# Kernel tuning notes

Hardware: AMD Instinct MI355X
Metric: run time of the kernel (lower is better)

The kernel has to match this reference:

```python
import jax, jax.numpy as jnp
import numpy as np

NBIN = 256
EPS = 1e-10


def _diffhist(img, hmin, hmax):
    # Soft (linear-interpolation) histogram, faithful to torch index_add version.
    img = img.ravel()
    keep = (img >= hmin) & (img <= hmax)
    dh = (hmax - hmin) / (NBIN - 1)
    x = (img - hmin) / dh
    idx = jnp.floor(x)
    d = x - idx  # fractional part, carries the gradient
    # zero-weight + clamped index instead of boolean compaction (jit-friendly)
    idx_i = jnp.where(keep, idx.astype(jnp.int32), 0)
    w0 = jnp.where(keep, 1.0 - d, 0.0)
    w1 = jnp.where(keep, d, 0.0)
    h = jnp.zeros(NBIN + 1, dtype=img.dtype)
    h = h.at[idx_i].add(w0).at[idx_i + 1].add(w1)
    return h[:NBIN]


def setup_inputs() -> dict:
    key = jax.random.key(0)
    k0, k1 = jax.random.split(key)
    shape = (4, 256, 256, 256)
    img0 = jax.random.normal(k0, shape, dtype=jnp.float32)
    img1 = jax.random.normal(k1, shape, dtype=jnp.float32)
    return {"img0": img0, "img1": img1}


def reference(img0, img1):
    min0 = jnp.min(img0)  # differentiable, like torch.min
    h0 = _diffhist(img0, min0, 0.0)
    h1 = _diffhist(img1, min0, 0.0)
    h0 = (h0 + EPS) / (h0.sum() + EPS)
    h1 = (h1 + EPS) / (h1.sum() + EPS)
    # KLDivLoss(log_target=True, reduction='mean'):
    #   mean( exp(target) * (target - input) )
    inp = jnp.log((h1 + EPS) / h1)
    tgt = jnp.log((h1 + EPS) / h0)
    return jnp.mean(jnp.exp(tgt) * (tgt - inp))
```

## Files before the change

### kernel.cpp

```cpp
#include <hip/hip_runtime.h>

#define NBIN 256
#define EPSF 1e-10f
#define DSCALE 4096.0f
#define DSCALE_INV (1.0 / 4096.0)
#define DMASK ((1ull << 40) - 1)

__device__ __forceinline__ unsigned enc_f32(float f) {
    unsigned u = __float_as_uint(f);
    return (u & 0x80000000u) ? ~u : (u ^ 0x80000000u);
}
__device__ __forceinline__ float dec_f32(unsigned e) {
    unsigned u = (e & 0x80000000u) ? (e ^ 0x80000000u) : ~e;
    return __uint_as_float(u);
}

__global__ void init_kernel(unsigned* ws_min, unsigned long long* gh) {
    if (threadIdx.x == 0) *ws_min = 0xFFFFFFFFu;
    for (int j = threadIdx.x; j < 2 * NBIN; j += blockDim.x) gh[j] = 0ull;
}

__global__ void __launch_bounds__(256) min_kernel(const float4* __restrict__ img0,
                                                  long n4, unsigned* ws_min) {
    long stride = (long)gridDim.x * blockDim.x;
    long i = (long)blockIdx.x * blockDim.x + threadIdx.x;
    float m = __int_as_float(0x7f800000);
    if (i < n4) {
        float4 cur = img0[i];
        long j = i + stride;
        for (; j < n4; j += stride) {
            float4 nxt = img0[j];
            m = fminf(m, fminf(fminf(cur.x, cur.y), fminf(cur.z, cur.w)));
            cur = nxt;
        }
        m = fminf(m, fminf(fminf(cur.x, cur.y), fminf(cur.z, cur.w)));
    }
    for (int off = 32; off; off >>= 1) m = fminf(m, __shfl_xor(m, off));
    __shared__ float sm[4];
    int lane = threadIdx.x & 63, wid = threadIdx.x >> 6;
    if (lane == 0) sm[wid] = m;
    __syncthreads();
    if (threadIdx.x == 0) {
        float bm = fminf(fminf(sm[0], sm[1]), fminf(sm[2], sm[3]));
        atomicMin(ws_min, enc_f32(bm));
    }
}

__device__ __forceinline__ void hadd(float v, float hmin, float inv_dh,
                                     unsigned* h, int lane) {
    bool keep = (v >= hmin) & (v <= 0.f);
    float x = (v - hmin) * inv_dh;
    x = fminf(fmaxf(x, 0.f), 255.f);
    float fi = floorf(x);
    int idx = (int)fi;
    unsigned di = __float2uint_rn((x - fi) * DSCALE);
    unsigned pv = keep ? ((1u << 24) | di) : 0u;
    idx = keep ? idx : lane;
    atomicAdd(&h[idx], pv);
}

__global__ void __launch_bounds__(256) hist_kernel(const float4* __restrict__ img0,
                                                   const float4* __restrict__ img1,
                                                   long n4, const unsigned* ws_min,
                                                   unsigned long long* __restrict__ gh) {
    __shared__ unsigned lh[4][2][NBIN];
    int tid = threadIdx.x;
    int wid = tid >> 6;
    int lane = tid & 63;
    unsigned* base = &lh[0][0][0];
    for (int j = tid; j < 4 * 2 * NBIN; j += 256) base[j] = 0u;
    __syncthreads();

    float hmin = dec_f32(*ws_min);
    float dh = (0.f - hmin) / (NBIN - 1);
    float inv_dh = 1.0f / dh;

    long stride = (long)gridDim.x * blockDim.x;
    unsigned* h0 = &lh[wid][0][0];
    unsigned* h1 = &lh[wid][1][0];

    long i = (long)blockIdx.x * blockDim.x + tid;
    if (i < n4) {
        float4 a = img0[i];
        float4 b = img1[i];
        long j = i + stride;
        for (; j < n4; j += stride) {
            float4 an = img0[j];
            float4 bn = img1[j];
            hadd(a.x, hmin, inv_dh, h0, lane);
            hadd(a.y, hmin, inv_dh, h0, lane);
            hadd(a.z, hmin, inv_dh, h0, lane);
            hadd(a.w, hmin, inv_dh, h0, lane);
            hadd(b.x, hmin, inv_dh, h1, lane);
            hadd(b.y, hmin, inv_dh, h1, lane);
            hadd(b.z, hmin, inv_dh, h1, lane);
            hadd(b.w, hmin, inv_dh, h1, lane);
            a = an;
            b = bn;
        }
        hadd(a.x, hmin, inv_dh, h0, lane);
        hadd(a.y, hmin, inv_dh, h0, lane);
        hadd(a.z, hmin, inv_dh, h0, lane);
        hadd(a.w, hmin, inv_dh, h0, lane);
        hadd(b.x, hmin, inv_dh, h1, lane);
        hadd(b.y, hmin, inv_dh, h1, lane);
        hadd(b.z, hmin, inv_dh, h1, lane);
        hadd(b.w, hmin, inv_dh, h1, lane);
    }
    __syncthreads();

    for (int b = tid; b < NBIN; b += 256) {
        unsigned long long c0 = 0, f0 = 0, c1 = 0, f1 = 0;
        for (int w = 0; w < 4; ++w) {
            unsigned p0 = lh[w][0][b];
            unsigned p1 = lh[w][1][b];
            c0 += p0 >> 24; f0 += p0 & 0xFFFFFFu;
            c1 += p1 >> 24; f1 += p1 & 0xFFFFFFu;
        }
        atomicAdd(&gh[b], (c0 << 40) | f0);
        atomicAdd(&gh[NBIN + b], (c1 << 40) | f1);
    }
}

__global__ void __launch_bounds__(256) kl_kernel(const unsigned long long* __restrict__ gh,
                                                 float* __restrict__ out) {
    int i = threadIdx.x;
    unsigned long long p0 = gh[i];
    unsigned long long p1 = gh[NBIN + i];
    unsigned long long q0 = (i > 0) ? gh[i - 1] : 0ull;
    unsigned long long q1 = (i > 0) ? gh[NBIN + i - 1] : 0ull;
    float h0 = (float)((double)(p0 >> 40) - (double)(p0 & DMASK) * DSCALE_INV
                       + (double)(q0 & DMASK) * DSCALE_INV);
    float h1 = (float)((double)(p1 >> 40) - (double)(p1 & DMASK) * DSCALE_INV
                       + (double)(q1 & DMASK) * DSCALE_INV);

    __shared__ float sw[4];
    int lane = i & 63, wid = i >> 6;

    float v = h0;
    for (int off = 32; off; off >>= 1) v += __shfl_xor(v, off);
    if (lane == 0) sw[wid] = v;
    __syncthreads();
    float s0 = sw[0] + sw[1] + sw[2] + sw[3];
    __syncthreads();

    v = h1;
    for (int off = 32; off; off >>= 1) v += __shfl_xor(v, off);
    if (lane == 0) sw[wid] = v;
    __syncthreads();
    float s1 = sw[0] + sw[1] + sw[2] + sw[3];
    __syncthreads();

    float a = (h0 + EPSF) / (s0 + EPSF);
    float b = (h1 + EPSF) / (s1 + EPSF);
    float tgt = logf((b + EPSF) / a);
    float inp = logf((b + EPSF) / b);
    float term = expf(tgt) * (tgt - inp);

    v = term;
    for (int off = 32; off; off >>= 1) v += __shfl_xor(v, off);
    if (lane == 0) sw[wid] = v;
    __syncthreads();
    if (i == 0) out[0] = (sw[0] + sw[1] + sw[2] + sw[3]) / (float)NBIN;
}

extern "C" void kernel_launch(void* const* d_in, const int* in_sizes, int n_in,
                              void* d_out, int out_size, void* d_ws, size_t ws_size,
                              hipStream_t stream) {
    const float* img0 = (const float*)d_in[0];
    const float* img1 = (const float*)d_in[1];
    float* out = (float*)d_out;
    unsigned* ws_min = (unsigned*)d_ws;
    unsigned long long* gh = (unsigned long long*)((char*)d_ws + 16);

    long n = (long)in_sizes[0];
    long n4 = n / 4;

    init_kernel<<<1, 256, 0, stream>>>(ws_min, gh);
    min_kernel<<<2048, 256, 0, stream>>>((const float4*)img0, n4, ws_min);
    hist_kernel<<<2048, 256, 0, stream>>>((const float4*)img0, (const float4*)img1,
                                          n4, ws_min, gh);
    kl_kernel<<<1, 256, 0, stream>>>(gh, out);
}
```

Baseline: 197.2 us.

## Queue histogram updates per lane and issue LDS atomics only when wave is full

Replaces the unconditional per-element LDS atomicAdd with a per-lane register FIFO of up to three packed entries (bin, image, fraction). A wave issues a full-width atomic only when every lane has a pending entry or some lane's queue is full, so out-of-range samples (roughly half the data) no longer cost a wasted atomic slot. This adds ballots, shifts and 64-bit queue bookkeeping per element, and clamps the fractional part to 12 bits.

```diff
diff --git a/kernel.cpp b/kernel.cpp
--- a/kernel.cpp
+++ b/kernel.cpp
@@ -5,6 +5,7 @@
 #define DSCALE 4096.0f
 #define DSCALE_INV (1.0 / 4096.0)
 #define DMASK ((1ull << 40) - 1)
+#define FULLM 0xFFFFFFFFFFFFFFFFull
 
 __device__ __forceinline__ unsigned enc_f32(float f) {
     unsigned u = __float_as_uint(f);
@@ -46,17 +47,36 @@
     }
 }
 
-__device__ __forceinline__ void hadd(float v, float hmin, float inv_dh,
-                                     unsigned* h, int lane) {
+__device__ __forceinline__ void fifo_issue(unsigned* tab, int lane,
+                                           unsigned long long& q, int& cnt) {
+    bool has = cnt > 0;
+    int sh = has ? 21 * (cnt - 1) : 0;
+    unsigned e = has ? (unsigned)((q >> sh) & 0x1FFFFFull) : 0u;
+    unsigned off = has ? (e >> 12) : (unsigned)lane;
+    unsigned pv = has ? ((1u << 24) | (e & 0xFFFu)) : 0u;
+    atomicAdd(&tab[off], pv);
+    cnt -= has ? 1 : 0;
+}
+
+__device__ __forceinline__ void slot(float v, float hmin, float inv_dh, int img,
+                                     unsigned* tab, int lane,
+                                     unsigned long long& q, int& cnt) {
     bool keep = (v >= hmin) & (v <= 0.f);
     float x = (v - hmin) * inv_dh;
     x = fminf(fmaxf(x, 0.f), 255.f);
     float fi = floorf(x);
     int idx = (int)fi;
     unsigned di = __float2uint_rn((x - fi) * DSCALE);
-    unsigned pv = keep ? ((1u << 24) | di) : 0u;
-    idx = keep ? idx : lane;
-    atomicAdd(&h[idx], pv);
+    di = di > 4095u ? 4095u : di;
+    unsigned entry = ((unsigned)((img << 8) | idx) << 12) | di;
+
+    bool pressure = keep && (cnt == 3);
+    unsigned long long ne = __ballot(cnt > 0);
+    if (__ballot(pressure) != 0ull || ne == FULLM) {
+        fifo_issue(tab, lane, q, cnt);
+    }
+    q = keep ? ((q << 21) | (unsigned long long)entry) : q;
+    cnt += keep ? 1 : 0;
 }
 
 __global__ void __launch_bounds__(256) hist_kernel(const float4* __restrict__ img0,
@@ -76,8 +96,10 @@
     float inv_dh = 1.0f / dh;
 
     long stride = (long)gridDim.x * blockDim.x;
-    unsigned* h0 = &lh[wid][0][0];
-    unsigned* h1 = &lh[wid][1][0];
+    unsigned* tab = &lh[wid][0][0];
+
+    unsigned long long q = 0ull;
+    int cnt = 0;
 
     long i = (long)blockIdx.x * blockDim.x + tid;
     if (i < n4) {
@@ -87,26 +109,27 @@
         for (; j < n4; j += stride) {
             float4 an = img0[j];
             float4 bn = img1[j];
-            hadd(a.x, hmin, inv_dh, h0, lane);
-            hadd(a.y, hmin, inv_dh, h0, lane);
-            hadd(a.z, hmin, inv_dh, h0, lane);
-            hadd(a.w, hmin, inv_dh, h0, lane);
-            hadd(b.x, hmin, inv_dh, h1, lane);
-            hadd(b.y, hmin, inv_dh, h1, lane);
-            hadd(b.z, hmin, inv_dh, h1, lane);
-            hadd(b.w, hmin, inv_dh, h1, lane);
+            slot(a.x, hmin, inv_dh, 0, tab, lane, q, cnt);
+            slot(a.y, hmin, inv_dh, 0, tab, lane, q, cnt);
+            slot(a.z, hmin, inv_dh, 0, tab, lane, q, cnt);
+            slot(a.w, hmin, inv_dh, 0, tab, lane, q, cnt);
+            slot(b.x, hmin, inv_dh, 1, tab, lane, q, cnt);
+            slot(b.y, hmin, inv_dh, 1, tab, lane, q, cnt);
+            slot(b.z, hmin, inv_dh, 1, tab, lane, q, cnt);
+            slot(b.w, hmin, inv_dh, 1, tab, lane, q, cnt);
             a = an;
             b = bn;
         }
-        hadd(a.x, hmin, inv_dh, h0, lane);
-        hadd(a.y, hmin, inv_dh, h0, lane);
-        hadd(a.z, hmin, inv_dh, h0, lane);
-        hadd(a.w, hmin, inv_dh, h0, lane);
-        hadd(b.x, hmin, inv_dh, h1, lane);
-        hadd(b.y, hmin, inv_dh, h1, lane);
-        hadd(b.z, hmin, inv_dh, h1, lane);
-        hadd(b.w, hmin, inv_dh, h1, lane);
-    }
+        slot(a.x, hmin, inv_dh, 0, tab, lane, q, cnt);
+        slot(a.y, hmin, inv_dh, 0, tab, lane, q, cnt);
+        slot(a.z, hmin, inv_dh, 0, tab, lane, q, cnt);
+        slot(a.w, hmin, inv_dh, 0, tab, lane, q, cnt);
+        slot(b.x, hmin, inv_dh, 1, tab, lane, q, cnt);
+        slot(b.y, hmin, inv_dh, 1, tab, lane, q, cnt);
+        slot(b.z, hmin, inv_dh, 1, tab, lane, q, cnt);
+        slot(b.w, hmin, inv_dh, 1, tab, lane, q, cnt);
+    }
+    for (int k = 0; k < 3; ++k) fifo_issue(tab, lane, q, cnt);
     __syncthreads();
 
     for (int b = tid; b < NBIN; b += 256) {
```

Result: faster. 181.9 us, median of 2 (-7.7%).

## Compact kept histogram entries via wave ballot ring before LDS atomics

Applied to the files above, without the earlier changes.

Replaces per-element LDS atomics (including dummy atomics for rejected values) with wave-level stream compaction into a per-wave LDS ring buffer, flushing 64 fully-populated atomics at a time. This is intended to cut the number of shared-memory atomics roughly in proportion to the rejected fraction. It adds ballot/mbcnt bookkeeping, extra LDS stores and loads, and clamps the fractional part to 12 bits.

```diff
diff --git a/kernel.cpp b/kernel.cpp
--- a/kernel.cpp
+++ b/kernel.cpp
@@ -1,6 +1,7 @@
 #include <hip/hip_runtime.h>
 
 #define NBIN 256
+#define RCAP 256
 #define EPSF 1e-10f
 #define DSCALE 4096.0f
 #define DSCALE_INV (1.0 / 4096.0)
@@ -46,24 +47,12 @@
     }
 }
 
-__device__ __forceinline__ void hadd(float v, float hmin, float inv_dh,
-                                     unsigned* h, int lane) {
-    bool keep = (v >= hmin) & (v <= 0.f);
-    float x = (v - hmin) * inv_dh;
-    x = fminf(fmaxf(x, 0.f), 255.f);
-    float fi = floorf(x);
-    int idx = (int)fi;
-    unsigned di = __float2uint_rn((x - fi) * DSCALE);
-    unsigned pv = keep ? ((1u << 24) | di) : 0u;
-    idx = keep ? idx : lane;
-    atomicAdd(&h[idx], pv);
-}
-
 __global__ void __launch_bounds__(256) hist_kernel(const float4* __restrict__ img0,
                                                    const float4* __restrict__ img1,
                                                    long n4, const unsigned* ws_min,
                                                    unsigned long long* __restrict__ gh) {
     __shared__ unsigned lh[4][2][NBIN];
+    __shared__ unsigned ring[4][RCAP];
     int tid = threadIdx.x;
     int wid = tid >> 6;
     int lane = tid & 63;
@@ -76,8 +65,32 @@
     float inv_dh = 1.0f / dh;
 
     long stride = (long)gridDim.x * blockDim.x;
-    unsigned* h0 = &lh[wid][0][0];
-    unsigned* h1 = &lh[wid][1][0];
+    unsigned* tab = &lh[wid][0][0];
+    unsigned* rg = &ring[wid][0];
+
+    unsigned head = 0, tail = 0;
+
+    auto slot = [&](float v, int img) {
+        bool keep = (v >= hmin) & (v <= 0.f);
+        float x = (v - hmin) * inv_dh;
+        x = fminf(fmaxf(x, 0.f), 255.f);
+        float fi = floorf(x);
+        int idx = (int)fi;
+        unsigned di = __float2uint_rn((x - fi) * DSCALE);
+        di = di > 4095u ? 4095u : di;
+        unsigned entry = ((unsigned)((img << 8) | idx) << 12) | di;
+
+        unsigned long long mask = __ballot(keep);
+        unsigned rank = __builtin_amdgcn_mbcnt_hi(
+            (unsigned)(mask >> 32), __builtin_amdgcn_mbcnt_lo((unsigned)mask, 0u));
+        if (keep) rg[(tail + rank) & (RCAP - 1)] = entry;
+        tail += (unsigned)__popcll(mask);
+        if (tail - head >= 64u) {
+            unsigned e = rg[(head + lane) & (RCAP - 1)];
+            atomicAdd(&tab[e >> 12], (1u << 24) | (e & 0xFFFu));
+            head += 64u;
+        }
+    };
 
     long i = (long)blockIdx.x * blockDim.x + tid;
     if (i < n4) {
@@ -87,25 +100,27 @@
         for (; j < n4; j += stride) {
             float4 an = img0[j];
             float4 bn = img1[j];
-            hadd(a.x, hmin, inv_dh, h0, lane);
-            hadd(a.y, hmin, inv_dh, h0, lane);
-            hadd(a.z, hmin, inv_dh, h0, lane);
-            hadd(a.w, hmin, inv_dh, h0, lane);
-            hadd(b.x, hmin, inv_dh, h1, lane);
-            hadd(b.y, hmin, inv_dh, h1, lane);
-            hadd(b.z, hmin, inv_dh, h1, lane);
-            hadd(b.w, hmin, inv_dh, h1, lane);
+            slot(a.x, 0); slot(a.y, 0); slot(a.z, 0); slot(a.w, 0);
+            slot(b.x, 1); slot(b.y, 1); slot(b.z, 1); slot(b.w, 1);
             a = an;
             b = bn;
         }
-        hadd(a.x, hmin, inv_dh, h0, lane);
-        hadd(a.y, hmin, inv_dh, h0, lane);
-        hadd(a.z, hmin, inv_dh, h0, lane);
-        hadd(a.w, hmin, inv_dh, h0, lane);
-        hadd(b.x, hmin, inv_dh, h1, lane);
-        hadd(b.y, hmin, inv_dh, h1, lane);
-        hadd(b.z, hmin, inv_dh, h1, lane);
-        hadd(b.w, hmin, inv_dh, h1, lane);
+        slot(a.x, 0); slot(a.y, 0); slot(a.z, 0); slot(a.w, 0);
+        slot(b.x, 1); slot(b.y, 1); slot(b.z, 1); slot(b.w, 1);
+    }
+    {
+        unsigned rem = tail - head;
+        if (lane < (int)rem) {
+            unsigned e = rg[(head + lane) & (RCAP - 1)];
+            atomicAdd(&tab[e >> 12], (1u << 24) | (e & 0xFFFu));
+        }
+        if (rem > 64u) {
+            unsigned r2 = rem - 64u;
+            if (lane < (int)r2) {
+                unsigned e = rg[(head + 64u + lane) & (RCAP - 1)];
+                atomicAdd(&tab[e >> 12], (1u << 24) | (e & 0xFFFu));
+            }
+        }
     }
     __syncthreads();
 
```

New measurement: 197.5 us. Within noise of the previous version (+0.2%).
